# Optimization experiments

Measured on AMD Instinct MI355X. Metric: run time of the kernel, lower is better.

Reference implementation:

```python
import jax, jax.numpy as jnp
import numpy as np

NEG_SLOPE = 0.1
K = 3  # kernel_size

def lrelu(x):
    return jnp.where(x >= 0, x, NEG_SLOPE * x)

def setup_inputs() -> dict:
    key = jax.random.key(0)
    ks = jax.random.split(key, 10)
    B, C, H, W = 16, 64, 128, 128
    DEG, RED = 512, 8
    s = 0.02
    return {
        "feat": jax.random.normal(ks[0], (B, C, H, W), jnp.float32),
        "deg": jax.random.normal(ks[1], (B, DEG, 8, 8), jnp.float32),
        # adaptive_size: Linear(deg_fsize -> C), no bias; torch weight [out,in]
        "W_size": jax.random.normal(ks[2], (C, DEG), jnp.float32) * s,
        # kernel net: Linear(C -> C//red), Linear(C//red -> C*K*K)
        "W_k1": jax.random.normal(ks[3], (C // RED, C), jnp.float32) * s,
        "W_k2": jax.random.normal(ks[4], (C * K * K, C // RED), jnp.float32) * s,
        # 1x1 conv C_in -> C_out with bias (stored as [out,in])
        "W_conv": jax.random.normal(ks[5], (C, C), jnp.float32) * s,
        "b_conv": jax.random.normal(ks[6], (C,), jnp.float32) * s,
        # CA layer: 1x1 conv deg_fsize -> C, then C -> C//red -> C
        "W_ac": jax.random.normal(ks[7], (C, DEG), jnp.float32) * s,
        "W_du1": jax.random.normal(ks[8], (C // RED, C), jnp.float32) * s,
        "W_du2": jax.random.normal(ks[9], (C, C // RED), jnp.float32) * s,
    }

def reference(feat, deg, W_size, W_k1, W_k2, W_conv, b_conv, W_ac, W_du1, W_du2):
    b, c, h, w = feat.shape
    # degradation pooled to a vector: AdaptiveAvgPool2d((1,1)) == mean over HW
    dvec = deg.mean(axis=(2, 3))                      # [B, deg_fsize]
    f = dvec @ W_size.T                               # [B, C]
    # per-sample dynamic depthwise kernels
    kern = lrelu(f @ W_k1.T) @ W_k2.T                 # [B, C*K*K]
    kern = kern.reshape(b * c, 1, K, K)               # [B*C, 1, K, K]
    out = jax.lax.conv_general_dilated(
        feat.reshape(1, b * c, h, w), kern,
        window_strides=(1, 1), padding=[((K - 1) // 2,) * 2] * 2,
        feature_group_count=b * c,
        dimension_numbers=("NCHW", "OIHW", "NCHW"))
    out = lrelu(out).reshape(b, c, h, w)
    # trailing 1x1 conv with bias
    out = jnp.einsum("bchw,oc->bohw", out, W_conv) + b_conv[None, :, None, None]
    # CA branch
    fa = dvec @ W_ac.T                                # [B, C]
    att = jax.nn.sigmoid(lrelu(fa @ W_du1.T) @ W_du2.T)  # [B, C_out]
    return out + feat * att[:, :, None, None]
```

## Files before the change

kernel.cpp:

```cpp
#include <hip/hip_runtime.h>
#include <math.h>

#define NEG_SLOPE 0.1f

typedef __attribute__((ext_vector_type(8))) short short8;
typedef __attribute__((ext_vector_type(4))) short short4v;
typedef __attribute__((ext_vector_type(4))) float floatx4;

__device__ __forceinline__ float lrelu(float x) { return x >= 0.0f ? x : NEG_SLOPE * x; }

__device__ __forceinline__ unsigned short f2bf(float x) {
  unsigned u = __float_as_uint(x);
  return (unsigned short)((u + 0x7fffu + ((u >> 16) & 1u)) >> 16);
}

__device__ __forceinline__ float wave_sum64(float v) {
  #pragma unroll
  for (int s = 32; s > 0; s >>= 1) v += __shfl_xor(v, s, 64);
  return v;
}

__global__ __launch_bounds__(256) void prep_kernel(
    const float* __restrict__ deg, const float* __restrict__ W_size,
    const float* __restrict__ W_k1, const float* __restrict__ W_k2,
    const float* __restrict__ W_ac, const float* __restrict__ W_du1,
    const float* __restrict__ W_du2, float* __restrict__ kern_ws,
    float* __restrict__ att_ws) {
  const int b = blockIdx.x;
  const int t = threadIdx.x;
  __shared__ float dvec[512];
  __shared__ float fbuf[64], fabuf[64];
  __shared__ float t1s[8], t2s[8];

  const float* degb = deg + (size_t)b * 32768;
  const int half = t & 1, row0 = t >> 1;
  #pragma unroll
  for (int u = 0; u < 4; ++u) {
    const int d = row0 + u * 128;
    const float* p = degb + (size_t)d * 64 + half * 32;
    float4 x0 = *(const float4*)(p);
    float4 x1 = *(const float4*)(p + 4);
    float4 x2 = *(const float4*)(p + 8);
    float4 x3 = *(const float4*)(p + 12);
    float4 x4 = *(const float4*)(p + 16);
    float4 x5 = *(const float4*)(p + 20);
    float4 x6 = *(const float4*)(p + 24);
    float4 x7 = *(const float4*)(p + 28);
    float s = (x0.x + x0.y + x0.z + x0.w) + (x1.x + x1.y + x1.z + x1.w) +
              (x2.x + x2.y + x2.z + x2.w) + (x3.x + x3.y + x3.z + x3.w) +
              (x4.x + x4.y + x4.z + x4.w) + (x5.x + x5.y + x5.z + x5.w) +
              (x6.x + x6.y + x6.z + x6.w) + (x7.x + x7.y + x7.z + x7.w);
    s += __shfl_xor(s, 1, 64);
    if (half == 0) dvec[d] = s * (1.0f / 64.0f);
  }
  __syncthreads();

  {
    const int c = t >> 2, q = t & 3;
    const float* w1 = W_size + (size_t)c * 512;
    const float* w2 = W_ac + (size_t)c * 512;
    float p1 = 0.0f, p2 = 0.0f;
    #pragma unroll 4
    for (int kk = 0; kk < 32; ++kk) {
      const int e = kk * 16 + q * 4;
      float4 d4 = *(const float4*)&dvec[e];
      float4 a4 = *(const float4*)(w1 + e);
      float4 b4 = *(const float4*)(w2 + e);
      p1 += d4.x * a4.x + d4.y * a4.y + d4.z * a4.z + d4.w * a4.w;
      p2 += d4.x * b4.x + d4.y * b4.y + d4.z * b4.z + d4.w * b4.w;
    }
    p1 += __shfl_xor(p1, 1, 64); p1 += __shfl_xor(p1, 2, 64);
    p2 += __shfl_xor(p2, 1, 64); p2 += __shfl_xor(p2, 2, 64);
    if (q == 0) { fbuf[c] = p1; fabuf[c] = p2; }
  }
  __syncthreads();

  const int wave = t >> 6, lane = t & 63;
  if (wave == 0) {
    float v = fbuf[lane];
    #pragma unroll
    for (int rr = 0; rr < 8; ++rr) {
      float p = wave_sum64(v * W_k1[rr * 64 + lane]);
      if (lane == 0) t1s[rr] = lrelu(p);
    }
  } else if (wave == 1) {
    float v = fabuf[lane];
    #pragma unroll
    for (int rr = 0; rr < 8; ++rr) {
      float p = wave_sum64(v * W_du1[rr * 64 + lane]);
      if (lane == 0) t2s[rr] = lrelu(p);
    }
  }
  __syncthreads();

  for (int i = t; i < 576; i += 256) {
    float4 wa0 = *(const float4*)&W_k2[i * 8];
    float4 wa1 = *(const float4*)&W_k2[i * 8 + 4];
    kern_ws[b * 576 + i] =
        t1s[0] * wa0.x + t1s[1] * wa0.y + t1s[2] * wa0.z + t1s[3] * wa0.w +
        t1s[4] * wa1.x + t1s[5] * wa1.y + t1s[6] * wa1.z + t1s[7] * wa1.w;
  }
  if (t < 64) {
    float4 wa0 = *(const float4*)&W_du2[t * 8];
    float4 wa1 = *(const float4*)&W_du2[t * 8 + 4];
    float s = t2s[0] * wa0.x + t2s[1] * wa0.y + t2s[2] * wa0.z + t2s[3] * wa0.w +
              t2s[4] * wa1.x + t2s[5] * wa1.y + t2s[6] * wa1.z + t2s[7] * wa1.w;
    att_ws[b * 64 + t] = 1.0f / (1.0f + expf(-s));
  }
}

__global__ __launch_bounds__(256, 5) void fused_kernel(
    const float* __restrict__ feat, const float* __restrict__ W_conv,
    const float* __restrict__ b_conv, const float* __restrict__ kern_ws,
    const float* __restrict__ att_ws, float* __restrict__ out) {
  const int bid = blockIdx.x;
  const int b = bid >> 7;
  const int h = bid & 127;

  const int t = threadIdx.x;

  __shared__ __align__(16) unsigned short zT[128 * 72];
  __shared__ __align__(16) unsigned short wt[64 * 72];
  __shared__ float ks[576];
  __shared__ float atts[64];
  __shared__ float bcs[64];

  {
    const int o = t >> 2;
    const int c0 = (t & 3) * 16;
    const float* wp = W_conv + o * 64 + c0;
    float4 a0 = *(const float4*)(wp);
    float4 a1 = *(const float4*)(wp + 4);
    float4 a2 = *(const float4*)(wp + 8);
    float4 a3 = *(const float4*)(wp + 12);
    const int sw = ((o >> 2) ^ (o >> 5)) & 7;
    short8 p0, p1;
    p0[0] = f2bf(a0.x); p0[1] = f2bf(a0.y); p0[2] = f2bf(a0.z); p0[3] = f2bf(a0.w);
    p0[4] = f2bf(a1.x); p0[5] = f2bf(a1.y); p0[6] = f2bf(a1.z); p0[7] = f2bf(a1.w);
    p1[0] = f2bf(a2.x); p1[1] = f2bf(a2.y); p1[2] = f2bf(a2.z); p1[3] = f2bf(a2.w);
    p1[4] = f2bf(a3.x); p1[5] = f2bf(a3.y); p1[6] = f2bf(a3.z); p1[7] = f2bf(a3.w);
    const int kc0 = ((c0 >> 3) + 0) ^ sw;
    const int kc1 = ((c0 >> 3) + 1) ^ sw;
    *(short8*)&wt[o * 72 + kc0 * 8] = p0;
    *(short8*)&wt[o * 72 + kc1 * 8] = p1;
  }
  for (int i = t; i < 576; i += 256) ks[i] = kern_ws[b * 576 + i];
  if (t < 64) { atts[t] = att_ws[b * 64 + t]; bcs[t] = b_conv[t]; }
  __syncthreads();

  const size_t base_b = (size_t)b * 64 * 128 * 128;
  const int lane = t & 63, wave = t >> 6;
  const int cq = t >> 5;
  const int gg = t & 31;
  const int w0 = gg * 4;
  const int swz = (gg ^ (gg >> 3)) & 7;
  const float4 zf4 = {0.f, 0.f, 0.f, 0.f};

  const bool hgt0 = (h > 0), hlt = (h < 127);
  const float* fbase = feat + base_b + (size_t)h * 128 + w0;

  #pragma unroll
  for (int it = 0; it < 2; ++it) {
    const int c0 = cq * 4 + it * 32;
    float4 top[4], mid[4], bot[4];
    #pragma unroll
    for (int j = 0; j < 4; ++j) {
      const float* p = fbase + (size_t)(c0 + j) * 16384;
      mid[j] = *(const float4*)p;
      top[j] = hgt0 ? *(const float4*)(p - 128) : zf4;
      bot[j] = hlt  ? *(const float4*)(p + 128) : zf4;
    }
    unsigned short sres[4][4];
    #pragma unroll
    for (int j = 0; j < 4; ++j) {
      const float* kv = &ks[(c0 + j) * 9];
      const float k0 = kv[0], k1 = kv[1], k2 = kv[2];
      const float k3 = kv[3], k4 = kv[4], k5 = kv[5];
      const float k6 = kv[6], k7 = kv[7], k8 = kv[8];
      float a0 = 0.f, a1 = 0.f, a2 = 0.f, a3 = 0.f;
      {
        float4 m = top[j];
        float lf = __shfl(m.w, lane - 1, 64); if (gg == 0)  lf = 0.f;
        float rt = __shfl(m.x, lane + 1, 64); if (gg == 31) rt = 0.f;
        a0 += k0 * lf  + k1 * m.x + k2 * m.y;
        a1 += k0 * m.x + k1 * m.y + k2 * m.z;
        a2 += k0 * m.y + k1 * m.z + k2 * m.w;
        a3 += k0 * m.z + k1 * m.w + k2 * rt;
      }
      {
        float4 m = mid[j];
        float lf = __shfl(m.w, lane - 1, 64); if (gg == 0)  lf = 0.f;
        float rt = __shfl(m.x, lane + 1, 64); if (gg == 31) rt = 0.f;
        a0 += k3 * lf  + k4 * m.x + k5 * m.y;
        a1 += k3 * m.x + k4 * m.y + k5 * m.z;
        a2 += k3 * m.y + k4 * m.z + k5 * m.w;
        a3 += k3 * m.z + k4 * m.w + k5 * rt;
      }
      {
        float4 m = bot[j];
        float lf = __shfl(m.w, lane - 1, 64); if (gg == 0)  lf = 0.f;
        float rt = __shfl(m.x, lane + 1, 64); if (gg == 31) rt = 0.f;
        a0 += k6 * lf  + k7 * m.x + k8 * m.y;
        a1 += k6 * m.x + k7 * m.y + k8 * m.z;
        a2 += k6 * m.y + k7 * m.z + k8 * m.w;
        a3 += k6 * m.z + k7 * m.w + k8 * rt;
      }
      sres[j][0] = f2bf(lrelu(a0));
      sres[j][1] = f2bf(lrelu(a1));
      sres[j][2] = f2bf(lrelu(a2));
      sres[j][3] = f2bf(lrelu(a3));
    }
    const int chunk = (cq >> 1) + it * 4;
    const int kcs = ((chunk ^ swz) * 8) + (cq & 1) * 4;
    #pragma unroll
    for (int i = 0; i < 4; ++i) {
      short4v sv;
      sv[0] = (short)sres[0][i]; sv[1] = (short)sres[1][i];
      sv[2] = (short)sres[2][i]; sv[3] = (short)sres[3][i];
      *(short4v*)&zT[(w0 + i) * 72 + kcs] = sv;
    }
  }
  __syncthreads();

  {
    const int r = lane & 15, q = lane >> 4;

    short8 az[2][2];
    #pragma unroll
    for (int wm2 = 0; wm2 < 2; ++wm2) {
      const int w = (wave * 2 + wm2) * 16 + r;
      const int sz = ((w >> 2) ^ (w >> 5)) & 7;
      #pragma unroll
      for (int ksp = 0; ksp < 2; ++ksp) {
        const int kc = (ksp * 4 + q) ^ sz;
        az[wm2][ksp] = *(const short8*)&zT[w * 72 + kc * 8];
      }
    }
    short8 bw[4][2];
    #pragma unroll
    for (int nt = 0; nt < 4; ++nt) {
      const int o = nt * 16 + r;
      const int so = ((o >> 2) ^ (o >> 5)) & 7;
      #pragma unroll
      for (int ksp = 0; ksp < 2; ++ksp) {
        const int kc = (ksp * 4 + q) ^ so;
        bw[nt][ksp] = *(const short8*)&wt[o * 72 + kc * 8];
      }
    }

    floatx4 acc[2][4];
    #pragma unroll
    for (int wm2 = 0; wm2 < 2; ++wm2)
      #pragma unroll
      for (int nt = 0; nt < 4; ++nt) acc[wm2][nt] = (floatx4){0.f, 0.f, 0.f, 0.f};

    #pragma unroll
    for (int wm2 = 0; wm2 < 2; ++wm2)
      #pragma unroll
      for (int nt = 0; nt < 4; ++nt)
        #pragma unroll
        for (int ksp = 0; ksp < 2; ++ksp)
          acc[wm2][nt] = __builtin_amdgcn_mfma_f32_16x16x32_bf16(
              az[wm2][ksp], bw[nt][ksp], acc[wm2][nt], 0, 0, 0);

    #pragma unroll
    for (int wm2 = 0; wm2 < 2; ++wm2) {
      const int wb = (wave * 2 + wm2) * 16 + q * 4;
      #pragma unroll
      for (int nt = 0; nt < 4; ++nt) {
        const int o = nt * 16 + r;
        const size_t off = base_b + (size_t)o * 16384 + (size_t)h * 128 + wb;
        float4 fv = *(const float4*)(feat + off);
        const float at = atts[o], bo = bcs[o];
        floatx4 a = acc[wm2][nt];
        float4 ov;
        ov.x = a[0] + bo + at * fv.x;
        ov.y = a[1] + bo + at * fv.y;
        ov.z = a[2] + bo + at * fv.z;
        ov.w = a[3] + bo + at * fv.w;
        *(float4*)(out + off) = ov;
      }
    }
  }
}

extern "C" void kernel_launch(void* const* d_in, const int* in_sizes, int n_in,
                              void* d_out, int out_size, void* d_ws, size_t ws_size,
                              hipStream_t stream) {
  const float* feat   = (const float*)d_in[0];
  const float* deg    = (const float*)d_in[1];
  const float* W_size = (const float*)d_in[2];
  const float* W_k1   = (const float*)d_in[3];
  const float* W_k2   = (const float*)d_in[4];
  const float* W_conv = (const float*)d_in[5];
  const float* b_conv = (const float*)d_in[6];
  const float* W_ac   = (const float*)d_in[7];
  const float* W_du1  = (const float*)d_in[8];
  const float* W_du2  = (const float*)d_in[9];
  float* out = (float*)d_out;

  float* kern_ws = (float*)d_ws;
  float* att_ws  = kern_ws + 16 * 576;

  prep_kernel<<<16, 256, 0, stream>>>(deg, W_size, W_k1, W_k2, W_ac, W_du1,
                                      W_du2, kern_ws, att_ws);
  fused_kernel<<<2048, 256, 0, stream>>>(feat, W_conv, b_conv, kern_ws, att_ws,
                                         out);
}
```

Measured before the change: 180.7 us.

## Issue all feature loads before shared-memory sync and prefetch residual before MFMA

Every global load of the 3-row feature stencil for both channel groups is now issued before the first barrier, so their latency overlaps the W_conv and kernel staging into shared memory. The residual feature values are prefetched ahead of the MFMA phase instead of being loaded in the epilogue, and B-fragments are loaded one at a time next to their MFMAs. Launch bounds drop from 5 to 4 blocks per CU to leave room for the extra live registers, trading occupancy for more memory-level parallelism.

Measured after the change: 184.6 us. +2.2%, slower.

```diff
diff --git a/kernel.cpp b/kernel.cpp
--- a/kernel.cpp
+++ b/kernel.cpp
@@ -109,7 +109,7 @@
   }
 }
 
-__global__ __launch_bounds__(256, 5) void fused_kernel(
+__global__ __launch_bounds__(256, 4) void fused_kernel(
     const float* __restrict__ feat, const float* __restrict__ W_conv,
     const float* __restrict__ b_conv, const float* __restrict__ kern_ws,
     const float* __restrict__ att_ws, float* __restrict__ out) {
@@ -146,7 +146,6 @@
   }
   for (int i = t; i < 576; i += 256) ks[i] = kern_ws[b * 576 + i];
   if (t < 64) { atts[t] = att_ws[b * 64 + t]; bcs[t] = b_conv[t]; }
-  __syncthreads();
 
   const size_t base_b = (size_t)b * 64 * 128 * 128;
   const int lane = t & 63, wave = t >> 6;
@@ -159,17 +158,23 @@
   const bool hgt0 = (h > 0), hlt = (h < 127);
   const float* fbase = feat + base_b + (size_t)h * 128 + w0;
 
+  float4 top[2][4], mid[2][4], bot[2][4];
   #pragma unroll
   for (int it = 0; it < 2; ++it) {
     const int c0 = cq * 4 + it * 32;
-    float4 top[4], mid[4], bot[4];
     #pragma unroll
     for (int j = 0; j < 4; ++j) {
       const float* p = fbase + (size_t)(c0 + j) * 16384;
-      mid[j] = *(const float4*)p;
-      top[j] = hgt0 ? *(const float4*)(p - 128) : zf4;
-      bot[j] = hlt  ? *(const float4*)(p + 128) : zf4;
-    }
+      mid[it][j] = *(const float4*)p;
+      top[it][j] = hgt0 ? *(const float4*)(p - 128) : zf4;
+      bot[it][j] = hlt  ? *(const float4*)(p + 128) : zf4;
+    }
+  }
+  __syncthreads();
+
+  #pragma unroll
+  for (int it = 0; it < 2; ++it) {
+    const int c0 = cq * 4 + it * 32;
     unsigned short sres[4][4];
     #pragma unroll
     for (int j = 0; j < 4; ++j) {
@@ -179,7 +184,7 @@
       const float k6 = kv[6], k7 = kv[7], k8 = kv[8];
       float a0 = 0.f, a1 = 0.f, a2 = 0.f, a3 = 0.f;
       {
-        float4 m = top[j];
+        float4 m = top[it][j];
         float lf = __shfl(m.w, lane - 1, 64); if (gg == 0)  lf = 0.f;
         float rt = __shfl(m.x, lane + 1, 64); if (gg == 31) rt = 0.f;
         a0 += k0 * lf  + k1 * m.x + k2 * m.y;
@@ -188,7 +193,7 @@
         a3 += k0 * m.z + k1 * m.w + k2 * rt;
       }
       {
-        float4 m = mid[j];
+        float4 m = mid[it][j];
         float lf = __shfl(m.w, lane - 1, 64); if (gg == 0)  lf = 0.f;
         float rt = __shfl(m.x, lane + 1, 64); if (gg == 31) rt = 0.f;
         a0 += k3 * lf  + k4 * m.x + k5 * m.y;
@@ -197,7 +202,7 @@
         a3 += k3 * m.z + k4 * m.w + k5 * rt;
       }
       {
-        float4 m = bot[j];
+        float4 m = bot[it][j];
         float lf = __shfl(m.w, lane - 1, 64); if (gg == 0)  lf = 0.f;
         float rt = __shfl(m.x, lane + 1, 64); if (gg == 31) rt = 0.f;
         a0 += k6 * lf  + k7 * m.x + k8 * m.y;
@@ -225,6 +230,18 @@
   {
     const int r = lane & 15, q = lane >> 4;
 
+    float4 fv[2][4];
+    #pragma unroll
+    for (int wm2 = 0; wm2 < 2; ++wm2) {
+      const int wb = (wave * 2 + wm2) * 16 + q * 4;
+      #pragma unroll
+      for (int nt = 0; nt < 4; ++nt) {
+        const int o = nt * 16 + r;
+        fv[wm2][nt] = *(const float4*)(feat + base_b + (size_t)o * 16384 +
+                                       (size_t)h * 128 + wb);
+      }
+    }
+
     short8 az[2][2];
     #pragma unroll
     for (int wm2 = 0; wm2 < 2; ++wm2) {
@@ -236,7 +253,13 @@
         az[wm2][ksp] = *(const short8*)&zT[w * 72 + kc * 8];
       }
     }
-    short8 bw[4][2];
+
+    floatx4 acc[2][4];
+    #pragma unroll
+    for (int wm2 = 0; wm2 < 2; ++wm2)
+      #pragma unroll
+      for (int nt = 0; nt < 4; ++nt) acc[wm2][nt] = (floatx4){0.f, 0.f, 0.f, 0.f};
+
     #pragma unroll
     for (int nt = 0; nt < 4; ++nt) {
       const int o = nt * 16 + r;
@@ -244,24 +267,13 @@
       #pragma unroll
       for (int ksp = 0; ksp < 2; ++ksp) {
         const int kc = (ksp * 4 + q) ^ so;
-        bw[nt][ksp] = *(const short8*)&wt[o * 72 + kc * 8];
-      }
-    }
-
-    floatx4 acc[2][4];
-    #pragma unroll
-    for (int wm2 = 0; wm2 < 2; ++wm2)
-      #pragma unroll
-      for (int nt = 0; nt < 4; ++nt) acc[wm2][nt] = (floatx4){0.f, 0.f, 0.f, 0.f};
-
-    #pragma unroll
-    for (int wm2 = 0; wm2 < 2; ++wm2)
-      #pragma unroll
-      for (int nt = 0; nt < 4; ++nt)
+        short8 bw = *(const short8*)&wt[o * 72 + kc * 8];
         #pragma unroll
-        for (int ksp = 0; ksp < 2; ++ksp)
+        for (int wm2 = 0; wm2 < 2; ++wm2)
           acc[wm2][nt] = __builtin_amdgcn_mfma_f32_16x16x32_bf16(
-              az[wm2][ksp], bw[nt][ksp], acc[wm2][nt], 0, 0, 0);
+              az[wm2][ksp], bw, acc[wm2][nt], 0, 0, 0);
+      }
+    }
 
     #pragma unroll
     for (int wm2 = 0; wm2 < 2; ++wm2) {
@@ -270,14 +282,14 @@
       for (int nt = 0; nt < 4; ++nt) {
         const int o = nt * 16 + r;
         const size_t off = base_b + (size_t)o * 16384 + (size_t)h * 128 + wb;
-        float4 fv = *(const float4*)(feat + off);
         const float at = atts[o], bo = bcs[o];
         floatx4 a = acc[wm2][nt];
+        float4 fvv = fv[wm2][nt];
         float4 ov;
-        ov.x = a[0] + bo + at * fv.x;
-        ov.y = a[1] + bo + at * fv.y;
-        ov.z = a[2] + bo + at * fv.z;
-        ov.w = a[3] + bo + at * fv.w;
+        ov.x = a[0] + bo + at * fvv.x;
+        ov.y = a[1] + bo + at * fvv.y;
+        ov.z = a[2] + bo + at * fvv.z;
+        ov.w = a[3] + bo + at * fvv.w;
         *(float4*)(out + off) = ov;
       }
     }
```
